# Kernel optimization log

Measured on AMD Instinct MI355X. Metric: run time of the kernel, lower is better.

## Reference

```python
import jax, jax.numpy as jnp
import numpy as np

THRESHOLD = 0.0  # default float threshold, non-learned path
SURROGATE_TAU = 0.1

@jax.custom_vjp
def jumprelu(x):
    # Forward: hard threshold x * 1[x > THRESHOLD]
    return x * (x > THRESHOLD).astype(x.dtype)

def _jumprelu_fwd(x):
    return jumprelu(x), x

def _jumprelu_bwd(x, g):
    # Smooth surrogate gradient of x * sigmoid(x/tau)
    tau = SURROGATE_TAU
    sig = jax.nn.sigmoid(x / tau)
    surrogate = sig + x * sig * (1.0 - sig) / tau
    return (g * surrogate,)

jumprelu.defvjp(_jumprelu_fwd, _jumprelu_bwd)

NUM_TRANSFORMS = 64
D_MODEL = 2048
RANK = 32
BATCH = 2048

def setup_inputs() -> dict:
    key = jax.random.key(0)
    kx, kv, ku, ke = jax.random.split(key, 4)
    scale = (1.0 / (D_MODEL * RANK)) ** 0.25
    x = jax.random.normal(kx, (BATCH, D_MODEL), dtype=jnp.float32)
    V = jax.random.normal(kv, (NUM_TRANSFORMS, RANK, D_MODEL), dtype=jnp.float32) * scale
    U = jax.random.normal(ku, (NUM_TRANSFORMS, D_MODEL, RANK), dtype=jnp.float32) * scale
    encoder = jax.random.normal(ke, (NUM_TRANSFORMS, D_MODEL), dtype=jnp.float32)
    encoder = encoder / jnp.linalg.norm(encoder, axis=1, keepdims=True)
    bias = jnp.full((NUM_TRANSFORMS,), -1.0, dtype=jnp.float32)
    return {"x": x, "V": V, "U": U, "encoder": encoder, "bias": bias}

def reference(x, V, U, encoder, bias):
    # pre_acts: (batch, num_transforms)
    pre_acts = x @ encoder.T - bias
    gate = jumprelu(pre_acts)
    # Vx: (n, b, r); UVx: (n, b, d)
    Vx = jnp.einsum('nrd,bd->nbr', V, x)
    UVx = jnp.einsum('ndr,nbr->nbd', U, Vx)
    gated = UVx * gate.T[:, :, None]
    output = gated.sum(axis=0)  # (batch, d_model)
    u_norms = jnp.linalg.norm(U.reshape(U.shape[0], -1), axis=1)
    v_norms = jnp.linalg.norm(V.reshape(V.shape[0], -1), axis=1)
    frobenius_norms = u_norms * v_norms / (D_MODEL * RANK) ** 0.5
    return (output, gate, frobenius_norms)
```

## Files before the change

### kernel.cpp

```cpp
#include <hip/hip_runtime.h>


#define D_MODEL 2048
#define BATCH   2048
#define NT      64
#define RANK    32

typedef __attribute__((ext_vector_type(8))) __bf16 bf16x8;
typedef __attribute__((ext_vector_type(4))) float  f32x4;

__device__ __forceinline__ unsigned short f2bf(float f) {
  unsigned int u = __builtin_bit_cast(unsigned int, f);
  u += 0x7FFFu + ((u >> 16) & 1u);
  return (unsigned short)(u >> 16);
}

__device__ __forceinline__ void gload_lds16(const void* g, void* l) {
  __builtin_amdgcn_global_load_lds(
      (const __attribute__((address_space(1))) unsigned int*)g,
      (__attribute__((address_space(3))) unsigned int*)l,
      16, 0, 0);
}


__device__ __forceinline__ void block_reduce_store(float ss, float* dst, int slot) {
  __shared__ float red[256];
  int t = threadIdx.x;
  red[t] = ss;
  __syncthreads();
  for (int s = 128; s > 0; s >>= 1) {
    if (t < s) red[t] += red[t + s];
    __syncthreads();
  }
  if (t == 0) dst[slot] = red[0];
}

__global__ void k_prep(const float4* __restrict__ x, const float4* __restrict__ enc,
                       const float4* __restrict__ V, const float4* __restrict__ U,
                       ushort4* __restrict__ xb, ushort4* __restrict__ encb,
                       ushort4* __restrict__ Vb, unsigned short* __restrict__ Ut,
                       float* __restrict__ partV, float* __restrict__ partU) {
  int bid = blockIdx.x, t = threadIdx.x;
  if (bid < 1024) {
#pragma unroll
    for (int it = 0; it < 4; ++it) {
      int i = bid * 1024 + it * 256 + t;
      float4 v = x[i];
      ushort4 o;
      o.x = f2bf(v.x); o.y = f2bf(v.y); o.z = f2bf(v.z); o.w = f2bf(v.w);
      xb[i] = o;
    }
  } else if (bid < 1152) {
    int i = (bid - 1024) * 256 + t;
    float4 v = enc[i];
    ushort4 o;
    o.x = f2bf(v.x); o.y = f2bf(v.y); o.z = f2bf(v.z); o.w = f2bf(v.w);
    encb[i] = o;
  } else if (bid < 1408) {
    int b = bid - 1152;
    size_t base4 = (size_t)b * 4096;
    float ss = 0.f;
    for (int it = 0; it < 16; ++it) {
      size_t idx = base4 + t + it * 256;
      float4 v = V[idx];
      ss += v.x * v.x + v.y * v.y + v.z * v.z + v.w * v.w;
      ushort4 o;
      o.x = f2bf(v.x); o.y = f2bf(v.y); o.z = f2bf(v.z); o.w = f2bf(v.w);
      Vb[idx] = o;
    }
    block_reduce_store(ss, partV, b);
  } else {
    int b = bid - 1408;
    int n = b >> 2;
    size_t base4 = (size_t)b * 4096;
    float ss = 0.f;
    for (int it = 0; it < 16; ++it) {
      size_t idx4 = base4 + t + it * 256;
      float4 v = U[idx4];
      ss += v.x * v.x + v.y * v.y + v.z * v.z + v.w * v.w;
      size_t e = idx4 * 4 - (size_t)n * (D_MODEL * RANK);
      int dcol = (int)(e >> 5);
      int r = (int)(e & 31);
      ushort4 o;
      o.x = f2bf(v.x); o.y = f2bf(v.y); o.z = f2bf(v.z); o.w = f2bf(v.w);
      *(ushort4*)(Ut + (size_t)dcol * 2048 + n * 32 + r) = o;
    }
    block_reduce_store(ss, partU, b);
  }
}

__global__ void k_gate_reduce(const float* __restrict__ part, const float* __restrict__ bias,
                              float* __restrict__ gate,
                              const float* __restrict__ pU, const float* __restrict__ pV,
                              float* __restrict__ frob) {
  int t = threadIdx.x;
  if (blockIdx.x == 0 && t < NT) {
    float su = pU[4 * t] + pU[4 * t + 1] + pU[4 * t + 2] + pU[4 * t + 3];
    float sv = pV[4 * t] + pV[4 * t + 1] + pV[4 * t + 2] + pV[4 * t + 3];
    frob[t] = sqrtf(su) * sqrtf(sv) * (1.0f / 256.0f);
  }
#pragma unroll
  for (int u = 0; u < 4; ++u) {
    int idx = blockIdx.x * 1024 + u * 256 + t;
    float s = 0.f;
#pragma unroll
    for (int z = 0; z < 8; ++z) s += part[(size_t)z * (BATCH * NT) + idx];
    float pre = s - bias[idx & (NT - 1)];
    gate[idx] = pre > 0.f ? pre : 0.f;
  }
}

template <int WGM, int WGN, int MI, int NJ, int EPI, int SWZ, int TEAMS>
__global__ __launch_bounds__(TEAMS * 256, 4)
void gemm_bt(const unsigned short* __restrict__ A,
             const unsigned short* __restrict__ Bt,
             const float* __restrict__ aux,
             unsigned short* __restrict__ outB,
             float* __restrict__ outF, int K, int klen) {
  constexpr int BM = WGM * MI * 16;
  constexpr int BN = WGN * NJ * 16;
  constexpr int RA = BM / 32;
  constexpr int RB = BN / 32;
  __shared__ __align__(16) unsigned short smem[TEAMS * (BM + BN) * 64];

  const int tid = threadIdx.x;
  const int w = tid >> 6;
  const int lane = tid & 63;
  const int quad = lane >> 4;
  const int l15 = lane & 15;
  const int team = w >> 2;
  const int wl = w & 3;
  const int wm = wl % WGM;
  const int wn = wl / WGM;

  unsigned short* As = smem + team * (BM + BN) * 64;
  unsigned short* Bs = As + BM * 64;

  int blockM, blockN, kbeg;
  if constexpr (SWZ) {
    const int lin = blockIdx.x;
    const int xcd = lin & 7;
    const int i = lin >> 3;
    blockM = (xcd & 1) * 8 + (i & 7);
    blockN = (xcd >> 1) * 8 + (i >> 3);
    kbeg = 0;
  } else {
    blockN = blockIdx.x;
    blockM = blockIdx.y;
    kbeg = blockIdx.z * klen;
  }
  const int kspan = klen / TEAMS;
  kbeg += team * kspan;

  const int lrow = lane >> 3;
  const int lq = (lane & 7) ^ lrow;
  const unsigned short* Ag = A + (size_t)(blockM * BM + lrow) * K + kbeg + lq * 8;
  const unsigned short* Bg = Bt + (size_t)(blockN * BN + lrow) * K + kbeg + lq * 8;

  const int pcs = (quad ^ (lane & 7)) * 16;
  const int rfA = wm * MI * 16 + l15;
  const int rfB = wn * NJ * 16 + l15;

  f32x4 acc[MI][NJ];
  const f32x4 z = {0.f, 0.f, 0.f, 0.f};
#pragma unroll
  for (int i = 0; i < MI; ++i)
#pragma unroll
    for (int j = 0; j < NJ; ++j) acc[i][j] = z;

  for (int k0 = 0; k0 < kspan; k0 += 64) {
#pragma unroll
    for (int j = 0; j < RA; ++j)
      gload_lds16(Ag + (size_t)((j * 4 + wl) * 8) * K + k0,
                  (char*)As + (j * 4 + wl) * 1024);
#pragma unroll
    for (int j = 0; j < RB; ++j)
      gload_lds16(Bg + (size_t)((j * 4 + wl) * 8) * K + k0,
                  (char*)Bs + (j * 4 + wl) * 1024);
    __syncthreads();
#pragma unroll
    for (int s = 0; s < 2; ++s) {
      bf16x8 af[MI], bfr[NJ];
#pragma unroll
      for (int i = 0; i < MI; ++i)
        af[i] = *(const bf16x8*)((const char*)As + (rfA + i * 16) * 128 + (pcs ^ (s << 6)));
#pragma unroll
      for (int j = 0; j < NJ; ++j)
        bfr[j] = *(const bf16x8*)((const char*)Bs + (rfB + j * 16) * 128 + (pcs ^ (s << 6)));
#pragma unroll
      for (int i = 0; i < MI; ++i)
#pragma unroll
        for (int j = 0; j < NJ; ++j)
          acc[i][j] = __builtin_amdgcn_mfma_f32_16x16x32_bf16(af[i], bfr[j], acc[i][j], 0, 0, 0);
    }
    __syncthreads();
  }

  if constexpr (TEAMS == 2) {
    float4* red = (float4*)smem;
    if (team == 1) {
#pragma unroll
      for (int i = 0; i < MI; ++i)
#pragma unroll
        for (int j = 0; j < NJ; ++j) {
          float4 v = {acc[i][j][0], acc[i][j][1], acc[i][j][2], acc[i][j][3]};
          red[((wl * MI + i) * NJ + j) * 64 + lane] = v;
        }
    }
    __syncthreads();
    if (team == 1) return;
#pragma unroll
    for (int i = 0; i < MI; ++i)
#pragma unroll
      for (int j = 0; j < NJ; ++j) {
        float4 r = red[((wl * MI + i) * NJ + j) * 64 + lane];
        acc[i][j][0] += r.x; acc[i][j][1] += r.y;
        acc[i][j][2] += r.z; acc[i][j][3] += r.w;
      }
  }

  const int row0 = blockM * BM + wm * MI * 16 + quad * 4;
  const int col0 = blockN * BN + wn * NJ * 16 + l15;
#pragma unroll
  for (int i = 0; i < MI; ++i) {
#pragma unroll
    for (int j = 0; j < NJ; ++j) {
      const int col = col0 + j * 16;
#pragma unroll
      for (int t = 0; t < 4; ++t) {
        const int row = row0 + i * 16 + t;
        float v = acc[i][j][t];
        if constexpr (EPI == 0) {
          float g = aux[(size_t)row * NT + (col >> 5)];
          outB[(size_t)row * 2048 + col] = f2bf(v * g);
        } else if constexpr (EPI == 1) {
          outF[(size_t)row * 2048 + col] = v;
        } else {
          outF[(size_t)blockIdx.z * (BATCH * NT) + (size_t)row * NT + col] = v;
        }
      }
    }
  }
}


extern "C" void kernel_launch(void* const* d_in, const int* in_sizes, int n_in,
                              void* d_out, int out_size, void* d_ws, size_t ws_size,
                              hipStream_t stream) {
  const float* x    = (const float*)d_in[0];
  const float* V    = (const float*)d_in[1];
  const float* U    = (const float*)d_in[2];
  const float* enc  = (const float*)d_in[3];
  const float* bias = (const float*)d_in[4];

  float* out  = (float*)d_out;
  float* gate = out + (size_t)BATCH * D_MODEL;
  float* frob = gate + (size_t)BATCH * NT;

  char* ws = (char*)d_ws;
  unsigned short* xb   = (unsigned short*)(ws);
  unsigned short* Vb   = (unsigned short*)(ws + (8u << 20));
  unsigned short* Ut   = (unsigned short*)(ws + (16u << 20));
  unsigned short* Yg   = (unsigned short*)(ws + (24u << 20));
  float* gatePart      = (float*)Yg;
  unsigned short* encb = (unsigned short*)(ws + (32u << 20));
  float* partU = (float*)(ws + (32u << 20) + 262144);
  float* partV = partU + 256;

  k_prep<<<1664, 256, 0, stream>>>((const float4*)x, (const float4*)enc,
                                   (const float4*)V, (const float4*)U,
                                   (ushort4*)xb, (ushort4*)encb, (ushort4*)Vb, Ut,
                                   partV, partU);

  gemm_bt<4, 1, 2, 4, 3, 0, 1><<<dim3(1, 16, 8), 256, 0, stream>>>(
      xb, encb, nullptr, nullptr, gatePart, D_MODEL, 256);
  k_gate_reduce<<<128, 256, 0, stream>>>(gatePart, bias, gate, partU, partV, frob);

  gemm_bt<2, 2, 4, 2, 0, 1, 2><<<dim3(512, 1, 1), 512, 0, stream>>>(
      xb, Vb, gate, Yg, nullptr, D_MODEL, D_MODEL);

  gemm_bt<2, 2, 4, 2, 1, 1, 2><<<dim3(512, 1, 1), 512, 0, stream>>>(
      Yg, Ut, nullptr, nullptr, out, D_MODEL, D_MODEL);
}
```

Measured before the change: 154.1 us.

## Use 4-team split-K blocks with wider N tiles and tree LDS reduction

The two large GEMMs now launch 256 blocks of 1024 threads with four K-split teams per block and a larger N tile (NJ 2→4), instead of 512 blocks of 512 threads with two teams. A new swizzle mode maps the smaller grid across XCDs, and a two-stage LDS tree reduction combines the four teams' partial accumulators. The aim is more operand reuse per block and more in-block parallelism over K. In exchange it uses more registers and LDS per block, adds extra barriers in the reduction, and leaves fewer blocks to spread across CUs.

```diff
diff --git a/kernel.cpp b/kernel.cpp
--- a/kernel.cpp
+++ b/kernel.cpp
@@ -137,13 +137,20 @@
   unsigned short* Bs = As + BM * 64;
 
   int blockM, blockN, kbeg;
-  if constexpr (SWZ) {
+  if constexpr (SWZ == 1) {
     const int lin = blockIdx.x;
     const int xcd = lin & 7;
     const int i = lin >> 3;
     blockM = (xcd & 1) * 8 + (i & 7);
     blockN = (xcd >> 1) * 8 + (i >> 3);
     kbeg = 0;
+  } else if constexpr (SWZ == 2) {
+    const int lin = blockIdx.x;
+    const int xcd = lin & 7;
+    const int i = lin >> 3;
+    blockM = (xcd & 1) * 8 + (i & 7);
+    blockN = (xcd >> 1) * 4 + (i >> 3);
+    kbeg = 0;
   } else {
     blockN = blockIdx.x;
     blockM = blockIdx.y;
@@ -196,24 +203,66 @@
     __syncthreads();
   }
 
+  float4* red = (float4*)smem;
+  const int rslot = ((wl * MI) * NJ) * 64 + lane;
   if constexpr (TEAMS == 2) {
-    float4* red = (float4*)smem;
     if (team == 1) {
 #pragma unroll
       for (int i = 0; i < MI; ++i)
 #pragma unroll
+        for (int j = 0; j < NJ; ++j)
+          red[rslot + (i * NJ + j) * 64] =
+              (float4){acc[i][j][0], acc[i][j][1], acc[i][j][2], acc[i][j][3]};
+    }
+    __syncthreads();
+    if (team == 1) return;
+#pragma unroll
+    for (int i = 0; i < MI; ++i)
+#pragma unroll
+      for (int j = 0; j < NJ; ++j) {
+        float4 r = red[rslot + (i * NJ + j) * 64];
+        acc[i][j][0] += r.x; acc[i][j][1] += r.y;
+        acc[i][j][2] += r.z; acc[i][j][3] += r.w;
+      }
+  } else if constexpr (TEAMS == 4) {
+    constexpr int SEC = 4 * MI * NJ * 64;
+    if (team == 1 || team == 3) {
+      float4* dst = red + (team >> 1) * SEC;
+#pragma unroll
+      for (int i = 0; i < MI; ++i)
+#pragma unroll
+        for (int j = 0; j < NJ; ++j)
+          dst[rslot + (i * NJ + j) * 64] =
+              (float4){acc[i][j][0], acc[i][j][1], acc[i][j][2], acc[i][j][3]};
+    }
+    __syncthreads();
+    if (team == 0 || team == 2) {
+      float4* src = red + (team >> 1) * SEC;
+#pragma unroll
+      for (int i = 0; i < MI; ++i)
+#pragma unroll
         for (int j = 0; j < NJ; ++j) {
-          float4 v = {acc[i][j][0], acc[i][j][1], acc[i][j][2], acc[i][j][3]};
-          red[((wl * MI + i) * NJ + j) * 64 + lane] = v;
+          float4 r = src[rslot + (i * NJ + j) * 64];
+          acc[i][j][0] += r.x; acc[i][j][1] += r.y;
+          acc[i][j][2] += r.z; acc[i][j][3] += r.w;
         }
     }
     __syncthreads();
-    if (team == 1) return;
+    if (team == 2) {
+#pragma unroll
+      for (int i = 0; i < MI; ++i)
+#pragma unroll
+        for (int j = 0; j < NJ; ++j)
+          red[rslot + (i * NJ + j) * 64] =
+              (float4){acc[i][j][0], acc[i][j][1], acc[i][j][2], acc[i][j][3]};
+    }
+    __syncthreads();
+    if (team != 0) return;
 #pragma unroll
     for (int i = 0; i < MI; ++i)
 #pragma unroll
       for (int j = 0; j < NJ; ++j) {
-        float4 r = red[((wl * MI + i) * NJ + j) * 64 + lane];
+        float4 r = red[rslot + (i * NJ + j) * 64];
         acc[i][j][0] += r.x; acc[i][j][1] += r.y;
         acc[i][j][2] += r.z; acc[i][j][3] += r.w;
       }
@@ -276,9 +325,9 @@
       xb, encb, nullptr, nullptr, gatePart, D_MODEL, 256);
   k_gate_reduce<<<128, 256, 0, stream>>>(gatePart, bias, gate, partU, partV, frob);
 
-  gemm_bt<2, 2, 4, 2, 0, 1, 2><<<dim3(512, 1, 1), 512, 0, stream>>>(
+  gemm_bt<2, 2, 4, 4, 0, 2, 4><<<dim3(256, 1, 1), 1024, 0, stream>>>(
       xb, Vb, gate, Yg, nullptr, D_MODEL, D_MODEL);
 
-  gemm_bt<2, 2, 4, 2, 1, 1, 2><<<dim3(512, 1, 1), 512, 0, stream>>>(
+  gemm_bt<2, 2, 4, 4, 1, 2, 4><<<dim3(256, 1, 1), 1024, 0, stream>>>(
       Yg, Ut, nullptr, nullptr, out, D_MODEL, D_MODEL);
 }
```

Result: slower. 161.1 us (+4.5%).

## Fuse encoder GEMM into V projection and split-K the U projection

Applied to the files above, without the earlier changes.

Appends the bf16 encoder rows after V so that a single GEMM produces both the rank projections and the gate pre-activations, with bias and ReLU applied in its epilogue. This removes the separate split-K encoder GEMM and its reduce kernel. Gating moves to a standalone elementwise kernel that rescales Y in place. The second GEMM is split along K into two bf16 partial outputs, which a new reduce kernel sums into fp32. The intent is fewer launches and better occupancy in the second GEMM, at the cost of extra global traffic and bf16 rounding of the partial sums.

```diff
diff --git a/kernel.cpp b/kernel.cpp
--- a/kernel.cpp
+++ b/kernel.cpp
@@ -5,6 +5,7 @@
 #define BATCH   2048
 #define NT      64
 #define RANK    32
+#define NBV     2048
 
 typedef __attribute__((ext_vector_type(8))) __bf16 bf16x8;
 typedef __attribute__((ext_vector_type(4))) float  f32x4;
@@ -13,6 +14,10 @@
   unsigned int u = __builtin_bit_cast(unsigned int, f);
   u += 0x7FFFu + ((u >> 16) & 1u);
   return (unsigned short)(u >> 16);
+}
+__device__ __forceinline__ float bf2f(unsigned short h) {
+  unsigned int u = (unsigned int)h << 16;
+  return __builtin_bit_cast(float, u);
 }
 
 __device__ __forceinline__ void gload_lds16(const void* g, void* l) {
@@ -37,8 +42,8 @@
 
 __global__ void k_prep(const float4* __restrict__ x, const float4* __restrict__ enc,
                        const float4* __restrict__ V, const float4* __restrict__ U,
-                       ushort4* __restrict__ xb, ushort4* __restrict__ encb,
-                       ushort4* __restrict__ Vb, unsigned short* __restrict__ Ut,
+                       ushort4* __restrict__ xb, ushort4* __restrict__ VbEnc,
+                       unsigned short* __restrict__ Ut,
                        float* __restrict__ partV, float* __restrict__ partU) {
   int bid = blockIdx.x, t = threadIdx.x;
   if (bid < 1024) {
@@ -55,7 +60,7 @@
     float4 v = enc[i];
     ushort4 o;
     o.x = f2bf(v.x); o.y = f2bf(v.y); o.z = f2bf(v.z); o.w = f2bf(v.w);
-    encb[i] = o;
+    VbEnc[1048576 + i] = o;
   } else if (bid < 1408) {
     int b = bid - 1152;
     size_t base4 = (size_t)b * 4096;
@@ -66,7 +71,7 @@
       ss += v.x * v.x + v.y * v.y + v.z * v.z + v.w * v.w;
       ushort4 o;
       o.x = f2bf(v.x); o.y = f2bf(v.y); o.z = f2bf(v.z); o.w = f2bf(v.w);
-      Vb[idx] = o;
+      VbEnc[idx] = o;
     }
     block_reduce_store(ss, partV, b);
   } else {
@@ -89,10 +94,9 @@
   }
 }
 
-__global__ void k_gate_reduce(const float* __restrict__ part, const float* __restrict__ bias,
-                              float* __restrict__ gate,
-                              const float* __restrict__ pU, const float* __restrict__ pV,
-                              float* __restrict__ frob) {
+__global__ void k_gate_apply(ushort4* __restrict__ Y, const float* __restrict__ gate,
+                             const float* __restrict__ pU, const float* __restrict__ pV,
+                             float* __restrict__ frob) {
   int t = threadIdx.x;
   if (blockIdx.x == 0 && t < NT) {
     float su = pU[4 * t] + pU[4 * t + 1] + pU[4 * t + 2] + pU[4 * t + 3];
@@ -100,13 +104,32 @@
     frob[t] = sqrtf(su) * sqrtf(sv) * (1.0f / 256.0f);
   }
 #pragma unroll
-  for (int u = 0; u < 4; ++u) {
-    int idx = blockIdx.x * 1024 + u * 256 + t;
-    float s = 0.f;
-#pragma unroll
-    for (int z = 0; z < 8; ++z) s += part[(size_t)z * (BATCH * NT) + idx];
-    float pre = s - bias[idx & (NT - 1)];
-    gate[idx] = pre > 0.f ? pre : 0.f;
+  for (int it = 0; it < 4; ++it) {
+    int c = blockIdx.x * 1024 + it * 256 + t;
+    int row = c >> 9;
+    int n = (c & 511) >> 3;
+    float g = gate[row * NT + n];
+    ushort4 y = Y[c];
+    y.x = f2bf(bf2f(y.x) * g);
+    y.y = f2bf(bf2f(y.y) * g);
+    y.z = f2bf(bf2f(y.z) * g);
+    y.w = f2bf(bf2f(y.w) * g);
+    Y[c] = y;
+  }
+}
+
+__global__ void k_out_reduce(const ushort4* __restrict__ P, float4* __restrict__ out) {
+#pragma unroll
+  for (int it = 0; it < 4; ++it) {
+    int c = blockIdx.x * 1024 + it * 256 + threadIdx.x;
+    ushort4 a = P[c];
+    ushort4 b = P[c + 1048576];
+    float4 o;
+    o.x = bf2f(a.x) + bf2f(b.x);
+    o.y = bf2f(a.y) + bf2f(b.y);
+    o.z = bf2f(a.z) + bf2f(b.z);
+    o.w = bf2f(a.w) + bf2f(b.w);
+    out[c] = o;
   }
 }
 
@@ -137,17 +160,20 @@
   unsigned short* Bs = As + BM * 64;
 
   int blockM, blockN, kbeg;
-  if constexpr (SWZ) {
+  if constexpr (SWZ == 2) {
     const int lin = blockIdx.x;
     const int xcd = lin & 7;
     const int i = lin >> 3;
     blockM = (xcd & 1) * 8 + (i & 7);
-    blockN = (xcd >> 1) * 8 + (i >> 3);
+    blockN = (xcd >> 1) * 4 + (i >> 3);
+    kbeg = blockIdx.z * klen;
+  } else {
+    const int lin = blockIdx.x;
+    const int xcd = lin & 7;
+    const int i = lin >> 3;
+    blockM = xcd * 2 + (i & 1);
+    blockN = i >> 1;
     kbeg = 0;
-  } else {
-    blockN = blockIdx.x;
-    blockM = blockIdx.y;
-    kbeg = blockIdx.z * klen;
   }
   const int kspan = klen / TEAMS;
   kbeg += team * kspan;
@@ -196,28 +222,26 @@
     __syncthreads();
   }
 
-  if constexpr (TEAMS == 2) {
-    float4* red = (float4*)smem;
-    if (team == 1) {
-#pragma unroll
-      for (int i = 0; i < MI; ++i)
-#pragma unroll
-        for (int j = 0; j < NJ; ++j) {
-          float4 v = {acc[i][j][0], acc[i][j][1], acc[i][j][2], acc[i][j][3]};
-          red[((wl * MI + i) * NJ + j) * 64 + lane] = v;
-        }
-    }
-    __syncthreads();
-    if (team == 1) return;
+  float4* red = (float4*)smem;
+  const int rslot = ((wl * MI) * NJ) * 64 + lane;
+  if (team == 1) {
 #pragma unroll
     for (int i = 0; i < MI; ++i)
 #pragma unroll
-      for (int j = 0; j < NJ; ++j) {
-        float4 r = red[((wl * MI + i) * NJ + j) * 64 + lane];
-        acc[i][j][0] += r.x; acc[i][j][1] += r.y;
-        acc[i][j][2] += r.z; acc[i][j][3] += r.w;
-      }
-  }
+      for (int j = 0; j < NJ; ++j)
+        red[rslot + (i * NJ + j) * 64] =
+            (float4){acc[i][j][0], acc[i][j][1], acc[i][j][2], acc[i][j][3]};
+  }
+  __syncthreads();
+  if (team == 1) return;
+#pragma unroll
+  for (int i = 0; i < MI; ++i)
+#pragma unroll
+    for (int j = 0; j < NJ; ++j) {
+      float4 r = red[rslot + (i * NJ + j) * 64];
+      acc[i][j][0] += r.x; acc[i][j][1] += r.y;
+      acc[i][j][2] += r.z; acc[i][j][3] += r.w;
+    }
 
   const int row0 = blockM * BM + wm * MI * 16 + quad * 4;
   const int col0 = blockN * BN + wn * NJ * 16 + l15;
@@ -230,13 +254,15 @@
       for (int t = 0; t < 4; ++t) {
         const int row = row0 + i * 16 + t;
         float v = acc[i][j][t];
-        if constexpr (EPI == 0) {
-          float g = aux[(size_t)row * NT + (col >> 5)];
-          outB[(size_t)row * 2048 + col] = f2bf(v * g);
-        } else if constexpr (EPI == 1) {
-          outF[(size_t)row * 2048 + col] = v;
+        if constexpr (EPI == 2) {
+          if (col < NBV) {
+            outB[(size_t)row * 2048 + col] = f2bf(v);
+          } else {
+            float pre = v - aux[col - NBV];
+            outF[(size_t)row * NT + (col - NBV)] = pre > 0.f ? pre : 0.f;
+          }
         } else {
-          outF[(size_t)blockIdx.z * (BATCH * NT) + (size_t)row * NT + col] = v;
+          outB[(size_t)blockIdx.z * (2048u * 2048u) + (size_t)row * 2048 + col] = f2bf(v);
         }
       }
     }
@@ -258,27 +284,26 @@
   float* frob = gate + (size_t)BATCH * NT;
 
   char* ws = (char*)d_ws;
-  unsigned short* xb   = (unsigned short*)(ws);
-  unsigned short* Vb   = (unsigned short*)(ws + (8u << 20));
-  unsigned short* Ut   = (unsigned short*)(ws + (16u << 20));
-  unsigned short* Yg   = (unsigned short*)(ws + (24u << 20));
-  float* gatePart      = (float*)Yg;
-  unsigned short* encb = (unsigned short*)(ws + (32u << 20));
-  float* partU = (float*)(ws + (32u << 20) + 262144);
+  unsigned short* xb    = (unsigned short*)(ws);
+  unsigned short* VbEnc = (unsigned short*)(ws + (8u << 20));
+  unsigned short* Ut    = (unsigned short*)(ws + (17u << 20));
+  unsigned short* Y     = (unsigned short*)(ws + (25u << 20));
+  unsigned short* P     = xb;
+  float* partU = (float*)(ws + (33u << 20));
   float* partV = partU + 256;
 
   k_prep<<<1664, 256, 0, stream>>>((const float4*)x, (const float4*)enc,
                                    (const float4*)V, (const float4*)U,
-                                   (ushort4*)xb, (ushort4*)encb, (ushort4*)Vb, Ut,
+                                   (ushort4*)xb, (ushort4*)VbEnc, Ut,
                                    partV, partU);
 
-  gemm_bt<4, 1, 2, 4, 3, 0, 1><<<dim3(1, 16, 8), 256, 0, stream>>>(
-      xb, encb, nullptr, nullptr, gatePart, D_MODEL, 256);
-  k_gate_reduce<<<128, 256, 0, stream>>>(gatePart, bias, gate, partU, partV, frob);
-
-  gemm_bt<2, 2, 4, 2, 0, 1, 2><<<dim3(512, 1, 1), 512, 0, stream>>>(
-      xb, Vb, gate, Yg, nullptr, D_MODEL, D_MODEL);
-
-  gemm_bt<2, 2, 4, 2, 1, 1, 2><<<dim3(512, 1, 1), 512, 0, stream>>>(
-      Yg, Ut, nullptr, nullptr, out, D_MODEL, D_MODEL);
-}
+  gemm_bt<2, 2, 4, 2, 2, 3, 2><<<dim3(528, 1, 1), 512, 0, stream>>>(
+      xb, VbEnc, bias, Y, gate, D_MODEL, D_MODEL);
+
+  k_gate_apply<<<1024, 256, 0, stream>>>((ushort4*)Y, gate, partU, partV, frob);
+
+  gemm_bt<2, 2, 4, 4, 5, 2, 2><<<dim3(256, 1, 2), 512, 0, stream>>>(
+      Y, Ut, nullptr, P, nullptr, D_MODEL, 1024);
+
+  k_out_reduce<<<1024, 256, 0, stream>>>((const ushort4*)P, (float4*)out);
+}
```

Result: slower. 174.2 us (+13.0%).

## Fold gate projection into prep kernel and frob norms into GEMM epilogue

Applied to the files above, without the earlier changes.

The bf16 split-K MFMA gate GEMM and its separate reduce kernel are removed. 128 extra blocks of the prep kernel now compute the gate pre-activations in fp32 SIMT dot products, which also drops the bf16 cast of the encoder. The Frobenius norm computation moves into the first large GEMM launch, cutting five launches to three. The risk is that the SIMT gate blocks do a 512-iteration loop with per-lane strided encoder loads, and they may form a long tail at the end of the prep kernel.

```diff
diff --git a/kernel.cpp b/kernel.cpp
--- a/kernel.cpp
+++ b/kernel.cpp
@@ -37,9 +37,11 @@
 
 __global__ void k_prep(const float4* __restrict__ x, const float4* __restrict__ enc,
                        const float4* __restrict__ V, const float4* __restrict__ U,
-                       ushort4* __restrict__ xb, ushort4* __restrict__ encb,
-                       ushort4* __restrict__ Vb, unsigned short* __restrict__ Ut,
-                       float* __restrict__ partV, float* __restrict__ partU) {
+                       const float* __restrict__ bias,
+                       ushort4* __restrict__ xb, ushort4* __restrict__ Vb,
+                       unsigned short* __restrict__ Ut,
+                       float* __restrict__ partV, float* __restrict__ partU,
+                       float* __restrict__ gate) {
   int bid = blockIdx.x, t = threadIdx.x;
   if (bid < 1024) {
 #pragma unroll
@@ -50,14 +52,8 @@
       o.x = f2bf(v.x); o.y = f2bf(v.y); o.z = f2bf(v.z); o.w = f2bf(v.w);
       xb[i] = o;
     }
-  } else if (bid < 1152) {
-    int i = (bid - 1024) * 256 + t;
-    float4 v = enc[i];
-    ushort4 o;
-    o.x = f2bf(v.x); o.y = f2bf(v.y); o.z = f2bf(v.z); o.w = f2bf(v.w);
-    encb[i] = o;
-  } else if (bid < 1408) {
-    int b = bid - 1152;
+  } else if (bid < 1280) {
+    int b = bid - 1024;
     size_t base4 = (size_t)b * 4096;
     float ss = 0.f;
     for (int it = 0; it < 16; ++it) {
@@ -69,8 +65,8 @@
       Vb[idx] = o;
     }
     block_reduce_store(ss, partV, b);
-  } else {
-    int b = bid - 1408;
+  } else if (bid < 1536) {
+    int b = bid - 1280;
     int n = b >> 2;
     size_t base4 = (size_t)b * 4096;
     float ss = 0.f;
@@ -86,42 +82,48 @@
       *(ushort4*)(Ut + (size_t)dcol * 2048 + n * 32 + r) = o;
     }
     block_reduce_store(ss, partU, b);
-  }
-}
-
-__global__ void k_gate_reduce(const float* __restrict__ part, const float* __restrict__ bias,
-                              float* __restrict__ gate,
-                              const float* __restrict__ pU, const float* __restrict__ pV,
-                              float* __restrict__ frob) {
-  int t = threadIdx.x;
-  if (blockIdx.x == 0 && t < NT) {
-    float su = pU[4 * t] + pU[4 * t + 1] + pU[4 * t + 2] + pU[4 * t + 3];
-    float sv = pV[4 * t] + pV[4 * t + 1] + pV[4 * t + 2] + pV[4 * t + 3];
-    frob[t] = sqrtf(su) * sqrtf(sv) * (1.0f / 256.0f);
-  }
-#pragma unroll
-  for (int u = 0; u < 4; ++u) {
-    int idx = blockIdx.x * 1024 + u * 256 + t;
-    float s = 0.f;
-#pragma unroll
-    for (int z = 0; z < 8; ++z) s += part[(size_t)z * (BATCH * NT) + idx];
-    float pre = s - bias[idx & (NT - 1)];
-    gate[idx] = pre > 0.f ? pre : 0.f;
-  }
-}
-
-template <int WGM, int WGN, int MI, int NJ, int EPI, int SWZ, int TEAMS>
-__global__ __launch_bounds__(TEAMS * 256, 4)
+  } else {
+    int b = bid - 1536;
+    int wv = t >> 6;
+    int n = t & 63;
+    int r0 = b * 16 + wv * 4;
+    const float4* xr = x + (size_t)r0 * 512;
+    const float4* er = enc + (size_t)n * 512;
+    float a0 = 0.f, a1 = 0.f, a2 = 0.f, a3 = 0.f;
+    for (int k = 0; k < 512; ++k) {
+      float4 e = er[k];
+      float4 p0 = xr[k];
+      float4 p1 = xr[512 + k];
+      float4 p2 = xr[1024 + k];
+      float4 p3 = xr[1536 + k];
+      a0 += p0.x * e.x + p0.y * e.y + p0.z * e.z + p0.w * e.w;
+      a1 += p1.x * e.x + p1.y * e.y + p1.z * e.z + p1.w * e.w;
+      a2 += p2.x * e.x + p2.y * e.y + p2.z * e.z + p2.w * e.w;
+      a3 += p3.x * e.x + p3.y * e.y + p3.z * e.z + p3.w * e.w;
+    }
+    float bi = bias[n];
+    a0 -= bi; a1 -= bi; a2 -= bi; a3 -= bi;
+    gate[(size_t)(r0 + 0) * NT + n] = a0 > 0.f ? a0 : 0.f;
+    gate[(size_t)(r0 + 1) * NT + n] = a1 > 0.f ? a1 : 0.f;
+    gate[(size_t)(r0 + 2) * NT + n] = a2 > 0.f ? a2 : 0.f;
+    gate[(size_t)(r0 + 3) * NT + n] = a3 > 0.f ? a3 : 0.f;
+  }
+}
+
+template <int WGM, int WGN, int MI, int NJ, int EPI>
+__global__ __launch_bounds__(512, 4)
 void gemm_bt(const unsigned short* __restrict__ A,
              const unsigned short* __restrict__ Bt,
              const float* __restrict__ aux,
              unsigned short* __restrict__ outB,
-             float* __restrict__ outF, int K, int klen) {
+             float* __restrict__ outF,
+             const float* __restrict__ pU, const float* __restrict__ pV,
+             float* __restrict__ frob, int K) {
   constexpr int BM = WGM * MI * 16;
   constexpr int BN = WGN * NJ * 16;
   constexpr int RA = BM / 32;
   constexpr int RB = BN / 32;
-  __shared__ __align__(16) unsigned short smem[TEAMS * (BM + BN) * 64];
+  __shared__ __align__(16) unsigned short smem[2 * (BM + BN) * 64];
 
   const int tid = threadIdx.x;
   const int w = tid >> 6;
@@ -133,24 +135,24 @@
   const int wm = wl % WGM;
   const int wn = wl / WGM;
 
+  if constexpr (EPI == 0) {
+    if (blockIdx.x == 0 && tid < NT) {
+      float su = pU[4 * tid] + pU[4 * tid + 1] + pU[4 * tid + 2] + pU[4 * tid + 3];
+      float sv = pV[4 * tid] + pV[4 * tid + 1] + pV[4 * tid + 2] + pV[4 * tid + 3];
+      frob[tid] = sqrtf(su) * sqrtf(sv) * (1.0f / 256.0f);
+    }
+  }
+
   unsigned short* As = smem + team * (BM + BN) * 64;
   unsigned short* Bs = As + BM * 64;
 
-  int blockM, blockN, kbeg;
-  if constexpr (SWZ) {
-    const int lin = blockIdx.x;
-    const int xcd = lin & 7;
-    const int i = lin >> 3;
-    blockM = (xcd & 1) * 8 + (i & 7);
-    blockN = (xcd >> 1) * 8 + (i >> 3);
-    kbeg = 0;
-  } else {
-    blockN = blockIdx.x;
-    blockM = blockIdx.y;
-    kbeg = blockIdx.z * klen;
-  }
-  const int kspan = klen / TEAMS;
-  kbeg += team * kspan;
+  const int lin = blockIdx.x;
+  const int xcd = lin & 7;
+  const int i0 = lin >> 3;
+  const int blockM = (xcd & 1) * 8 + (i0 & 7);
+  const int blockN = (xcd >> 1) * 8 + (i0 >> 3);
+  const int kspan = K / 2;
+  const int kbeg = team * kspan;
 
   const int lrow = lane >> 3;
   const int lq = (lane & 7) ^ lrow;
@@ -196,28 +198,26 @@
     __syncthreads();
   }
 
-  if constexpr (TEAMS == 2) {
-    float4* red = (float4*)smem;
-    if (team == 1) {
-#pragma unroll
-      for (int i = 0; i < MI; ++i)
-#pragma unroll
-        for (int j = 0; j < NJ; ++j) {
-          float4 v = {acc[i][j][0], acc[i][j][1], acc[i][j][2], acc[i][j][3]};
-          red[((wl * MI + i) * NJ + j) * 64 + lane] = v;
-        }
-    }
-    __syncthreads();
-    if (team == 1) return;
+  float4* red = (float4*)smem;
+  const int rslot = ((wl * MI) * NJ) * 64 + lane;
+  if (team == 1) {
 #pragma unroll
     for (int i = 0; i < MI; ++i)
 #pragma unroll
-      for (int j = 0; j < NJ; ++j) {
-        float4 r = red[((wl * MI + i) * NJ + j) * 64 + lane];
-        acc[i][j][0] += r.x; acc[i][j][1] += r.y;
-        acc[i][j][2] += r.z; acc[i][j][3] += r.w;
-      }
-  }
+      for (int j = 0; j < NJ; ++j)
+        red[rslot + (i * NJ + j) * 64] =
+            (float4){acc[i][j][0], acc[i][j][1], acc[i][j][2], acc[i][j][3]};
+  }
+  __syncthreads();
+  if (team == 1) return;
+#pragma unroll
+  for (int i = 0; i < MI; ++i)
+#pragma unroll
+    for (int j = 0; j < NJ; ++j) {
+      float4 r = red[rslot + (i * NJ + j) * 64];
+      acc[i][j][0] += r.x; acc[i][j][1] += r.y;
+      acc[i][j][2] += r.z; acc[i][j][3] += r.w;
+    }
 
   const int row0 = blockM * BM + wm * MI * 16 + quad * 4;
   const int col0 = blockN * BN + wn * NJ * 16 + l15;
@@ -233,10 +233,8 @@
         if constexpr (EPI == 0) {
           float g = aux[(size_t)row * NT + (col >> 5)];
           outB[(size_t)row * 2048 + col] = f2bf(v * g);
-        } else if constexpr (EPI == 1) {
+        } else {
           outF[(size_t)row * 2048 + col] = v;
-        } else {
-          outF[(size_t)blockIdx.z * (BATCH * NT) + (size_t)row * NT + col] = v;
         }
       }
     }
@@ -258,27 +256,21 @@
   float* frob = gate + (size_t)BATCH * NT;
 
   char* ws = (char*)d_ws;
-  unsigned short* xb   = (unsigned short*)(ws);
-  unsigned short* Vb   = (unsigned short*)(ws + (8u << 20));
-  unsigned short* Ut   = (unsigned short*)(ws + (16u << 20));
-  unsigned short* Yg   = (unsigned short*)(ws + (24u << 20));
-  float* gatePart      = (float*)Yg;
-  unsigned short* encb = (unsigned short*)(ws + (32u << 20));
-  float* partU = (float*)(ws + (32u << 20) + 262144);
+  unsigned short* xb = (unsigned short*)(ws);
+  unsigned short* Vb = (unsigned short*)(ws + (8u << 20));
+  unsigned short* Ut = (unsigned short*)(ws + (16u << 20));
+  unsigned short* Yg = (unsigned short*)(ws + (24u << 20));
+  float* partU = (float*)(ws + (32u << 20));
   float* partV = partU + 256;
 
   k_prep<<<1664, 256, 0, stream>>>((const float4*)x, (const float4*)enc,
-                                   (const float4*)V, (const float4*)U,
-                                   (ushort4*)xb, (ushort4*)encb, (ushort4*)Vb, Ut,
-                                   partV, partU);
-
-  gemm_bt<4, 1, 2, 4, 3, 0, 1><<<dim3(1, 16, 8), 256, 0, stream>>>(
-      xb, encb, nullptr, nullptr, gatePart, D_MODEL, 256);
-  k_gate_reduce<<<128, 256, 0, stream>>>(gatePart, bias, gate, partU, partV, frob);
-
-  gemm_bt<2, 2, 4, 2, 0, 1, 2><<<dim3(512, 1, 1), 512, 0, stream>>>(
-      xb, Vb, gate, Yg, nullptr, D_MODEL, D_MODEL);
-
-  gemm_bt<2, 2, 4, 2, 1, 1, 2><<<dim3(512, 1, 1), 512, 0, stream>>>(
-      Yg, Ut, nullptr, nullptr, out, D_MODEL, D_MODEL);
-}
+                                   (const float4*)V, (const float4*)U, bias,
+                                   (ushort4*)xb, (ushort4*)Vb, Ut,
+                                   partV, partU, gate);
+
+  gemm_bt<2, 2, 4, 2, 0><<<dim3(512), 512, 0, stream>>>(
+      xb, Vb, gate, Yg, nullptr, partU, partV, frob, D_MODEL);
+
+  gemm_bt<2, 2, 4, 2, 1><<<dim3(512), 512, 0, stream>>>(
+      Yg, Ut, nullptr, nullptr, out, nullptr, nullptr, nullptr, D_MODEL);
+}
```

After: 275.4 us. 78.7% more time.
